# Kernel optimization log

Hardware: AMD Instinct MI355X
Metric: run time of the kernel (lower is better)

Reference implementation:

```python
import jax, jax.numpy as jnp
import numpy as np

N_NODES = 10000
N_EDGES = 50000
N_GRAPHS = 64
NODE_DIM = 32
EDGE_DIM = 16
HID = 64
EDGE_HID = 128
OUT_DIM = 1
T_STEPS = 3       # message-passing rounds
S2S_STEPS = 6     # Set2Set processing steps


def setup_inputs() -> dict:
    key = jax.random.key(0)
    ks = jax.random.split(key, 24)
    def w(k, shape, scale):
        return (jax.random.normal(k, shape, dtype=jnp.float32) * scale)
    inp = {}
    inp["node_features"] = jax.random.normal(ks[0], (N_NODES, NODE_DIM), dtype=jnp.float32)
    inp["edge_features"] = jax.random.normal(ks[1], (N_EDGES, EDGE_DIM), dtype=jnp.float32)
    inp["edge_index"] = jax.random.randint(ks[2], (2, N_EDGES), 0, N_NODES, dtype=jnp.int32)
    # sorted, fully-covering graph assignment (nodes of each graph are contiguous)
    inp["batch_indices"] = ((jnp.arange(N_NODES) * N_GRAPHS) // N_NODES).astype(jnp.int32)
    # input projection
    inp["W_proj"] = w(ks[3], (NODE_DIM, HID), 1.0 / np.sqrt(NODE_DIM))
    inp["b_proj"] = jnp.zeros((HID,), jnp.float32)
    # edge network MLP: edge_dim -> edge_hid -> hid*hid
    inp["W_e1"] = w(ks[4], (EDGE_DIM, EDGE_HID), 1.0 / np.sqrt(EDGE_DIM))
    inp["b_e1"] = jnp.zeros((EDGE_HID,), jnp.float32)
    inp["W_e2"] = w(ks[5], (EDGE_HID, HID * HID), 0.01)
    inp["b_e2"] = jnp.zeros((HID * HID,), jnp.float32)
    # GRU cell (torch layout: 3*hid rows = r,z,n)
    inp["W_gih"] = w(ks[6], (3 * HID, HID), 1.0 / np.sqrt(HID))
    inp["W_ghh"] = w(ks[7], (3 * HID, HID), 1.0 / np.sqrt(HID))
    inp["b_gih"] = jnp.zeros((3 * HID,), jnp.float32)
    inp["b_ghh"] = jnp.zeros((3 * HID,), jnp.float32)
    # LSTM cell (torch layout: 4*hid rows = i,f,g,o), input 2*hid
    inp["W_lih"] = w(ks[8], (4 * HID, 2 * HID), 1.0 / np.sqrt(HID))
    inp["W_lhh"] = w(ks[9], (4 * HID, HID), 1.0 / np.sqrt(HID))
    inp["b_lih"] = jnp.zeros((4 * HID,), jnp.float32)
    inp["b_lhh"] = jnp.zeros((4 * HID,), jnp.float32)
    # readout MLP: 2*hid -> hid -> out
    inp["W_m1"] = w(ks[10], (2 * HID, HID), 1.0 / np.sqrt(2 * HID))
    inp["b_m1"] = jnp.zeros((HID,), jnp.float32)
    inp["W_m2"] = w(ks[11], (HID, OUT_DIM), 1.0 / np.sqrt(HID))
    inp["b_m2"] = jnp.zeros((OUT_DIM,), jnp.float32)
    return inp


def _scatter_softmax(e, idx, n_seg):
    mx = jax.ops.segment_max(e, idx, num_segments=n_seg)
    ex = jnp.exp(e - mx[idx])
    s = jax.ops.segment_sum(ex, idx, num_segments=n_seg)
    return ex / (s[idx] + 1e-16)


def _mpnn_forward(node_features, edge_features, edge_index, batch_indices,
                  W_proj, b_proj, W_e1, b_e1, W_e2, b_e2,
                  W_gih, W_ghh, b_gih, b_ghh,
                  W_lih, W_lhh, b_lih, b_lhh,
                  W_m1, b_m1, W_m2, b_m2):
    n_nodes = node_features.shape[0]
    dst = edge_index[0]  # receiving node v
    src = edge_index[1]  # sending node w

    # input projection
    h = node_features @ W_proj + b_proj                       # (N, H)

    # edge network: per-edge transformation matrix A(e_vw) (depends only on edge feats)
    A = jax.nn.relu(edge_features @ W_e1 + b_e1) @ W_e2 + b_e2
    A = A.reshape(-1, HID, HID)                               # (E, H, H)

    # T rounds: gather senders, per-edge bmm, scatter-add to receivers, GRU update
    for _ in range(T_STEPS):
        msgs = jnp.einsum('eij,ej->ei', A, h[src])            # (E, H)
        m = jax.ops.segment_sum(msgs, dst, num_segments=n_nodes)
        gx = m @ W_gih.T + b_gih                              # (N, 3H)
        gh = h @ W_ghh.T + b_ghh
        xr, xz, xn = jnp.split(gx, 3, axis=-1)
        hr, hz, hn = jnp.split(gh, 3, axis=-1)
        r = jax.nn.sigmoid(xr + hr)
        z = jax.nn.sigmoid(xz + hz)
        n = jnp.tanh(xn + r * hn)
        h = (1.0 - z) * n + z * h

    # Set2Set readout
    hs = jnp.zeros((N_GRAPHS, HID), h.dtype)
    cs = jnp.zeros((N_GRAPHS, HID), h.dtype)
    rs = jnp.zeros((N_GRAPHS, HID), h.dtype)
    for _ in range(S2S_STEPS):
        q = hs[batch_indices]                                 # (N, H)
        e = jnp.sum(h * q, axis=-1)                           # (N,)
        a = _scatter_softmax(e, batch_indices, N_GRAPHS)
        rs = jax.ops.segment_sum(a[:, None] * h, batch_indices, num_segments=N_GRAPHS)
        x = jnp.concatenate([hs, rs], axis=-1)                # (G, 2H)
        gates = x @ W_lih.T + b_lih + hs @ W_lhh.T + b_lhh    # (G, 4H)
        i, f, g, o = jnp.split(gates, 4, axis=-1)
        cs = jax.nn.sigmoid(f) * cs + jax.nn.sigmoid(i) * jnp.tanh(g)
        hs = jax.nn.sigmoid(o) * jnp.tanh(cs)
    ge = jnp.concatenate([hs, rs], axis=-1)                   # (G, 2H)
    return jax.nn.relu(ge @ W_m1 + b_m1) @ W_m2 + b_m2        # (G, out)


def reference(node_features, edge_features, edge_index, batch_indices,
              W_proj, b_proj, W_e1, b_e1, W_e2, b_e2,
              W_gih, W_ghh, b_gih, b_ghh,
              W_lih, W_lhh, b_lih, b_lhh,
              W_m1, b_m1, W_m2, b_m2):
    return _mpnn_forward(node_features, edge_features, edge_index, batch_indices,
                         W_proj, b_proj, W_e1, b_e1, W_e2, b_e2,
                         W_gih, W_ghh, b_gih, b_ghh,
                         W_lih, W_lhh, b_lih, b_lhh,
                         W_m1, b_m1, W_m2, b_m2)
```

## Files before the change

### kernel.cpp

```cpp
#include <hip/hip_runtime.h>

#define N_NODES   10000
#define N_EDGES   50000
#define N_GRAPHS  64
#define NODE_DIM  32
#define EDGE_DIM  16
#define HID       64
#define EHID      128
#define T_STEPS   3
#define S2S_STEPS 6
#define TMB       5

typedef _Float16 half_t;
typedef _Float16 f16x8 __attribute__((ext_vector_type(8)));
typedef float    f32x4 __attribute__((ext_vector_type(4)));

__device__ __forceinline__ float sigf(float x){ return 1.0f/(1.0f + expf(-x)); }

__global__ void k_zero(float* p, int n){
  int i = blockIdx.x*256 + threadIdx.x;
  if (i < n) p[i] = 0.0f;
}

__global__ void k_proj(const float* __restrict__ nf, const float* __restrict__ Wp,
                       const float* __restrict__ bp, float* __restrict__ h){
  int idx = blockIdx.x*256 + threadIdx.x;
  if (idx >= N_NODES*HID) return;
  int n = idx >> 6;
  int c = idx & 63;
  float acc = bp[c];
  const float* row = nf + (size_t)n*NODE_DIM;
  for (int j = 0; j < NODE_DIM; ++j)
    acc = fmaf(row[j], Wp[j*HID + c], acc);
  h[idx] = acc;
}

__global__ void k_tw2(const float* __restrict__ W2, float* __restrict__ Mm){
  int idx = blockIdx.x*256 + threadIdx.x;
  if (idx >= 64*8192) return;
  int j = idx >> 13; int o = idx & 8191; int k = o >> 6; int i = o & 63;
  Mm[idx] = W2[(size_t)k*4096 + i*64 + j];
}

__global__ void k_w2bt(const float* __restrict__ W2, half_t* __restrict__ BT){
  int idx = blockIdx.x*256 + threadIdx.x;
  if (idx >= 512*2*64*8) return;
  int j    = idx & 7;
  int lane = (idx >> 3) & 63;
  int tk   = (idx >> 9) & 1;
  int tn   = idx >> 10;
  int k = tk*32 + ((lane >> 4) << 3) + j;
  int o = tn*16 + (lane & 15);
  BT[idx] = (half_t)W2[(size_t)(o >> 6)*4096 + (o & 63)*64 + k];
}

__global__ void k_prep(const float* __restrict__ h, const float* __restrict__ be2,
                       float* __restrict__ m, float* __restrict__ bhp,
                       half_t* __restrict__ AT){
  int idx = blockIdx.x*256 + threadIdx.x;
  if (idx >= N_NODES*HID) return;
  m[idx] = 0.0f;
  int n = idx >> 6, i = idx & 63;
  float acc = 0.0f;
  const float* row = be2 + (size_t)i*64;
  const float* hr  = h + (size_t)n*64;
  for (int j = 0; j < 64; ++j)
    acc = fmaf(row[j], hr[j], acc);
  bhp[idx] = acc;
  int j    = idx & 7;
  int lane = (idx >> 3) & 63;
  int tk   = (idx >> 9) & 1;
  int tm   = idx >> 10;
  int mrow = tm*16 + (lane & 15);
  int k    = tk*32 + ((lane >> 4) << 3) + j;
  AT[idx] = (half_t)h[(size_t)mrow*64 + k];
}

__global__ void k_twg(const float* __restrict__ Wg, const float* __restrict__ Wh,
                      float* __restrict__ WgT, float* __restrict__ WhT){
  int idx = blockIdx.x*256 + threadIdx.x;
  if (idx >= 192*64) return;
  int row = idx >> 6;
  int j   = idx & 63;
  WgT[j*192 + row] = Wg[(size_t)row*64 + j];
  WhT[j*192 + row] = Wh[(size_t)row*64 + j];
}

__global__ void k_ehid(const float* __restrict__ ef, const float* __restrict__ W1,
                       const float* __restrict__ b1, float* __restrict__ Hid){
  int idx = blockIdx.x*256 + threadIdx.x;
  if (idx >= N_EDGES*EHID) return;
  int e = idx >> 7, c = idx & 127;
  float acc = b1[c];
  const float* er = ef + (size_t)e*EDGE_DIM;
  for (int j = 0; j < EDGE_DIM; ++j)
    acc = fmaf(er[j], W1[j*EHID + c], acc);
  Hid[idx] = fmaxf(acc, 0.0f);
}

__global__ void k_ehid16(const float* __restrict__ ef, const float* __restrict__ W1,
                         const float* __restrict__ b1, half_t* __restrict__ Hid16){
  int idx = blockIdx.x*256 + threadIdx.x;
  if (idx >= N_EDGES*EHID) return;
  int e = idx >> 7, c = idx & 127;
  float acc = b1[c];
  const float* er = ef + (size_t)e*EDGE_DIM;
  for (int j = 0; j < EDGE_DIM; ++j)
    acc = fmaf(er[j], W1[j*EHID + c], acc);
  Hid16[idx] = (half_t)fmaxf(acc, 0.0f);
}

__global__ void k_bh(const float* __restrict__ h, const float* __restrict__ be2,
                     float* __restrict__ bh){
  int idx = blockIdx.x*256 + threadIdx.x;
  if (idx >= N_NODES*HID) return;
  int n = idx >> 6, i = idx & 63;
  float acc = 0.0f;
  const float* row = be2 + (size_t)i*64;
  const float* hr  = h + (size_t)n*64;
  for (int j = 0; j < 64; ++j)
    acc = fmaf(row[j], hr[j], acc);
  bh[idx] = acc;
}

__global__ void k_hist(const int* __restrict__ ids, int* __restrict__ deg){
  int e = blockIdx.x*256 + threadIdx.x;
  if (e >= N_EDGES) return;
  atomicAdd(&deg[ids[e]], 1);
}

__global__ void k_scan(const int* __restrict__ deg, int* __restrict__ rowptr,
                       int* __restrict__ cursor){
  __shared__ int part[256];
  int t = threadIdx.x;
  int base = t*40;
  int s = 0;
  for (int i = 0; i < 40; ++i){
    int idx = base + i;
    if (idx < N_NODES) s += deg[idx];
  }
  part[t] = s;
  __syncthreads();
  for (int off = 1; off < 256; off <<= 1){
    int v = (t >= off) ? part[t - off] : 0;
    __syncthreads();
    part[t] += v;
    __syncthreads();
  }
  int run = (t > 0) ? part[t - 1] : 0;
  for (int i = 0; i < 40; ++i){
    int idx = base + i;
    if (idx < N_NODES){
      rowptr[idx] = run;
      cursor[idx] = run;
      run += deg[idx];
    }
  }
  if (t == 255) rowptr[N_NODES] = run;
}

__global__ void k_scatter(const int* __restrict__ ids, int* __restrict__ cursor,
                          int* __restrict__ csr){
  int e = blockIdx.x*256 + threadIdx.x;
  if (e >= N_EDGES) return;
  int v = ids[e];
  int pos = atomicAdd(&cursor[v], 1);
  csr[pos] = e;
}

__global__ __launch_bounds__(256, 2)
void MPNN_55705725829535_kernel(const half_t* __restrict__ AT,
                                const half_t* __restrict__ BT,
                                const int* __restrict__ rowptr,
                                const int* __restrict__ csr,
                                const int* __restrict__ ei,
                                const half_t* __restrict__ Hid16,
                                const float* __restrict__ bh,
                                float* __restrict__ m){
  __shared__ half_t Ct[16][2][520];
  __shared__ int edgW[4][4][16];
  __shared__ int dstW[4][4][16];
  int wv   = threadIdx.x >> 6;
  int lane = threadIdx.x & 63;
  int quad = lane >> 4;
  int colb = lane & 15;
  int tmg = blockIdx.x;
  int q   = blockIdx.y;
  int kh  = blockIdx.z;

  f16x8 B0r[2][8], B1r[2][8];
  #pragma unroll
  for (int ktl = 0; ktl < 2; ++ktl)
    #pragma unroll
    for (int jj = 0; jj < 8; ++jj){
      int ke = (kh*2 + ktl)*32 + wv*8 + jj;
      const f16x8* Bb = (const f16x8*)BT + (size_t)(ke*4 + q)*128;
      B0r[ktl][jj] = Bb[lane];
      B1r[ktl][jj] = Bb[64 + lane];
    }

  for (int tt = 0; tt < TMB; ++tt){
    int tm = tmg*TMB + tt;
    const f16x8* Ab = (const f16x8*)AT + (size_t)tm*128;
    f16x8 a0 = Ab[lane];
    f16x8 a1 = Ab[64 + lane];

    {
      int nodeL = wv*4 + quad;
      int sL = tm*16 + nodeL;
      int begL = rowptr[sL];
      int endL = rowptr[sL + 1];
      int eL = (colb < endL - begL) ? csr[begL + colb] : -1;
      edgW[wv][quad][colb] = eL;
      dstW[wv][quad][colb] = (eL >= 0) ? ei[eL] : -1;
    }

    #pragma unroll
    for (int ktl = 0; ktl < 2; ++ktl){
      f32x4 acc[8];
      #pragma unroll
      for (int jj = 0; jj < 8; ++jj){
        acc[jj][0]=0.f; acc[jj][1]=0.f; acc[jj][2]=0.f; acc[jj][3]=0.f;
      }
      #pragma unroll
      for (int jj = 0; jj < 8; ++jj){
        acc[jj] = __builtin_amdgcn_mfma_f32_16x16x32_f16(a0, B0r[ktl][jj], acc[jj], 0, 0, 0);
        acc[jj] = __builtin_amdgcn_mfma_f32_16x16x32_f16(a1, B1r[ktl][jj], acc[jj], 0, 0, 0);
      }
      #pragma unroll
      for (int r = 0; r < 4; ++r){
        int node = quad*4 + r;
        f16x8 v;
        #pragma unroll
        for (int jj = 0; jj < 8; ++jj) v[jj] = (half_t)acc[jj][r];
        *(f16x8*)&Ct[node][ktl][(wv*16 + colb)*8] = v;
      }
    }
    __syncthreads();

    for (int c = 0; c < 4; ++c){
      int node = wv*4 + c;
      int s = tm*16 + node;
      int beg  = rowptr[s];
      int endp = rowptr[s + 1];
      if (beg == endp) continue;
      f16x8 B0 = *(const f16x8*)&Ct[node][0][lane*8];
      f16x8 B1 = *(const f16x8*)&Ct[node][1][lane*8];
      float bhc = (kh == 0) ? bh[(size_t)s*64 + q*16 + colb] : 0.0f;
      int gn0 = endp - beg; if (gn0 > 16) gn0 = 16;
      {
        f16x8 A0, A1;
        int e = (colb < gn0) ? edgW[wv][c][colb] : -1;
        if (e >= 0){
          const f16x8* Hb = (const f16x8*)(Hid16 + (size_t)e*128) + quad;
          A0 = Hb[(kh*2 + 0)*4];
          A1 = Hb[(kh*2 + 1)*4];
        } else {
          #pragma unroll
          for (int p = 0; p < 8; ++p){ A0[p] = (half_t)0; A1[p] = (half_t)0; }
        }
        f32x4 acc;
        acc[0]=0.f; acc[1]=0.f; acc[2]=0.f; acc[3]=0.f;
        acc = __builtin_amdgcn_mfma_f32_16x16x32_f16(A0, B0, acc, 0, 0, 0);
        acc = __builtin_amdgcn_mfma_f32_16x16x32_f16(A1, B1, acc, 0, 0, 0);
        #pragma unroll
        for (int r = 0; r < 4; ++r){
          int jrow = quad*4 + r;
          if (jrow < gn0){
            int d = dstW[wv][c][jrow];
            atomicAdd(&m[(size_t)d*64 + q*16 + colb], acc[r] + bhc);
          }
        }
      }
      for (int gbeg = beg + 16; gbeg < endp; gbeg += 16){
        int gn = endp - gbeg; if (gn > 16) gn = 16;
        if (lane < 16){
          int e2 = (lane < gn) ? csr[gbeg + lane] : -1;
          edgW[wv][c][lane] = e2;
          dstW[wv][c][lane] = (e2 >= 0) ? ei[e2] : -1;
        }
        f16x8 A0, A1;
        int e = (colb < gn) ? edgW[wv][c][colb] : -1;
        if (e >= 0){
          const f16x8* Hb = (const f16x8*)(Hid16 + (size_t)e*128) + quad;
          A0 = Hb[(kh*2 + 0)*4];
          A1 = Hb[(kh*2 + 1)*4];
        } else {
          #pragma unroll
          for (int p = 0; p < 8; ++p){ A0[p] = (half_t)0; A1[p] = (half_t)0; }
        }
        f32x4 acc;
        acc[0]=0.f; acc[1]=0.f; acc[2]=0.f; acc[3]=0.f;
        acc = __builtin_amdgcn_mfma_f32_16x16x32_f16(A0, B0, acc, 0, 0, 0);
        acc = __builtin_amdgcn_mfma_f32_16x16x32_f16(A1, B1, acc, 0, 0, 0);
        #pragma unroll
        for (int r = 0; r < 4; ++r){
          int jrow = quad*4 + r;
          if (jrow < gn){
            int d = dstW[wv][c][jrow];
            atomicAdd(&m[(size_t)d*64 + q*16 + colb], acc[r] + bhc);
          }
        }
      }
    }
    __syncthreads();
  }
}

__global__ void k_cgemm(const float* __restrict__ h, const float* __restrict__ Mm,
                        half_t* __restrict__ C, int lo, int hi){
  __shared__ float hs[16][64];
  int n0 = lo + blockIdx.x*16;
  int o0 = blockIdx.y*256 + threadIdx.x;
  for (int idx = threadIdx.x; idx < 16*64; idx += 256){
    int nn = idx >> 6, j = idx & 63;
    int node = n0 + nn;
    hs[nn][j] = (node < hi) ? h[(size_t)node*64 + j] : 0.0f;
  }
  __syncthreads();
  float acc0[16], acc1[16];
  #pragma unroll
  for (int nn = 0; nn < 16; ++nn){ acc0[nn] = 0.0f; acc1[nn] = 0.0f; }
  for (int j4 = 0; j4 < 16; ++j4){
    const float* M0 = Mm + (size_t)(j4*4)*8192;
    float a0 = M0[o0],            b0 = M0[o0 + 4096];
    float a1 = M0[8192 + o0],     b1 = M0[8192 + o0 + 4096];
    float a2 = M0[2*8192 + o0],   b2 = M0[2*8192 + o0 + 4096];
    float a3 = M0[3*8192 + o0],   b3 = M0[3*8192 + o0 + 4096];
    #pragma unroll
    for (int nn = 0; nn < 16; ++nn){
      float4 hv = *(const float4*)&hs[nn][j4*4];
      acc0[nn] = fmaf(hv.x, a0, acc0[nn]);
      acc1[nn] = fmaf(hv.x, b0, acc1[nn]);
      acc0[nn] = fmaf(hv.y, a1, acc0[nn]);
      acc1[nn] = fmaf(hv.y, b1, acc1[nn]);
      acc0[nn] = fmaf(hv.z, a2, acc0[nn]);
      acc1[nn] = fmaf(hv.z, b2, acc1[nn]);
      acc0[nn] = fmaf(hv.w, a3, acc0[nn]);
      acc1[nn] = fmaf(hv.w, b3, acc1[nn]);
    }
  }
  #pragma unroll
  for (int nn = 0; nn < 16; ++nn){
    int node = n0 + nn;
    if (node < hi){
      half_t* Cr = C + (size_t)(node - lo)*8192;
      Cr[o0]        = (half_t)acc0[nn];
      Cr[o0 + 4096] = (half_t)acc1[nn];
    }
  }
}

__global__ void k_msg_csr(const int* __restrict__ rowptr,
                          const int* __restrict__ csr,
                          const int* __restrict__ ei,
                          const float* __restrict__ Hid,
                          const half_t* __restrict__ C,
                          const float* __restrict__ bh,
                          float* __restrict__ m, int lo, int hi){
  __shared__ float hidL[4][8][128];
  int wave = threadIdx.x >> 6;
  int lane = threadIdx.x & 63;
  int s = lo + blockIdx.x*4 + wave;
  if (s >= hi) return;
  int beg = rowptr[s];
  int endp = rowptr[s + 1];
  if (beg == endp) return;
  float bhv = bh[(size_t)s*64 + lane];
  const half_t* Cb = C + (size_t)(s - lo)*8192 + lane;
  float (*hl)[128] = hidL[wave];
  for (int gbeg = beg; gbeg < endp; gbeg += 8){
    int gn = endp - gbeg; if (gn > 8) gn = 8;
    int dsts[8];
    int e0 = csr[gbeg];
    #pragma unroll
    for (int j = 0; j < 8; ++j){
      int e = (j < gn) ? csr[gbeg + j] : e0;
      dsts[j] = ei[e];
      hl[j][lane]      = Hid[(size_t)e*128 + lane];
      hl[j][lane + 64] = Hid[(size_t)e*128 + 64 + lane];
    }
    float acc[8];
    #pragma unroll
    for (int j = 0; j < 8; ++j) acc[j] = 0.0f;
    #pragma unroll 4
    for (int k = 0; k < 128; ++k){
      float c = (float)Cb[k*64];
      #pragma unroll
      for (int j = 0; j < 8; ++j)
        acc[j] = fmaf(hl[j][k], c, acc[j]);
    }
    for (int j = 0; j < gn; ++j)
      atomicAdd(&m[(size_t)dsts[j]*64 + lane], acc[j] + bhv);
  }
}

__global__ void k_msg_fb(const int* __restrict__ ei, const float* __restrict__ ef,
                         const float* __restrict__ W1, const float* __restrict__ b1,
                         const float* __restrict__ W2, const float* __restrict__ be2,
                         const float* __restrict__ h, float* __restrict__ m){
  __shared__ float HidL[EHID];
  __shared__ __align__(16) float hsL[HID];
  int e = blockIdx.x;
  int t = threadIdx.x;
  int src = ei[N_EDGES + e];
  int dst = ei[e];
  {
    float a0 = b1[t];
    float a1 = b1[t + 64];
    const float* er = ef + (size_t)e*EDGE_DIM;
    for (int j = 0; j < EDGE_DIM; ++j){
      float ev = er[j];
      a0 = fmaf(ev, W1[j*EHID + t],      a0);
      a1 = fmaf(ev, W1[j*EHID + t + 64], a1);
    }
    HidL[t]      = fmaxf(a0, 0.0f);
    HidL[t + 64] = fmaxf(a1, 0.0f);
    hsL[t] = h[(size_t)src*64 + t];
  }
  __syncthreads();
  float acc = 0.0f;
  for (int k = 0; k < EHID; ++k){
    float s = HidL[k];
    if (s != 0.0f){
      const float* w = W2 + (size_t)k*4096 + t*64;
      float partial = 0.0f;
      for (int j = 0; j < 64; ++j)
        partial = fmaf(hsL[j], w[j], partial);
      acc = fmaf(s, partial, acc);
    }
  }
  {
    const float* w = be2 + (size_t)t*64;
    for (int j = 0; j < 64; ++j)
      acc = fmaf(hsL[j], w[j], acc);
  }
  atomicAdd(&m[(size_t)dst*64 + t], acc);
}

__global__ void k_gru(float* __restrict__ h, const float* __restrict__ m,
                      const float* __restrict__ WgT, const float* __restrict__ WhT,
                      const float* __restrict__ bg, const float* __restrict__ bhb){
  __shared__ float mld[16][64];
  __shared__ float hld[16][64];
  int t  = threadIdx.x;
  int i  = t & 63;
  int wv = t >> 6;
  int n0 = blockIdx.x*16;
  for (int idx = t; idx < 16*64; idx += 256){
    int nn = idx >> 6, j = idx & 63;
    int node = n0 + nn;
    mld[nn][j] = m[(size_t)node*64 + j];
    hld[nn][j] = h[(size_t)node*64 + j];
  }
  __syncthreads();
  float xr[4], xz[4], xn[4], hr[4], hz[4], hn[4];
  #pragma unroll
  for (int c = 0; c < 4; ++c){
    xr[c] = bg[i];  xz[c] = bg[64 + i];  xn[c] = bg[128 + i];
    hr[c] = bhb[i]; hz[c] = bhb[64 + i]; hn[c] = bhb[128 + i];
  }
  for (int j = 0; j < 64; ++j){
    const float* wg = WgT + j*192;
    const float* wh = WhT + j*192;
    float wgr = wg[i], wgz = wg[64 + i], wgn = wg[128 + i];
    float whr = wh[i], whz = wh[64 + i], whn = wh[128 + i];
    #pragma unroll
    for (int c = 0; c < 4; ++c){
      int nn = wv*4 + c;
      float mj = mld[nn][j];
      float hj = hld[nn][j];
      xr[c] = fmaf(mj, wgr, xr[c]);
      xz[c] = fmaf(mj, wgz, xz[c]);
      xn[c] = fmaf(mj, wgn, xn[c]);
      hr[c] = fmaf(hj, whr, hr[c]);
      hz[c] = fmaf(hj, whz, hz[c]);
      hn[c] = fmaf(hj, whn, hn[c]);
    }
  }
  #pragma unroll
  for (int c = 0; c < 4; ++c){
    int nn = wv*4 + c;
    float r  = sigf(xr[c] + hr[c]);
    float z  = sigf(xz[c] + hz[c]);
    float nv = tanhf(xn[c] + r*hn[c]);
    h[(size_t)(n0 + nn)*64 + i] = (1.0f - z)*nv + z*hld[nn][i];
  }
}

__global__ void k_s2s(const float* __restrict__ h,
                      const float* __restrict__ Wli, const float* __restrict__ Wlh,
                      const float* __restrict__ bli, const float* __restrict__ blh,
                      const float* __restrict__ Wm1, const float* __restrict__ bm1,
                      const float* __restrict__ Wm2, const float* __restrict__ bm2,
                      float* __restrict__ out){
  __shared__ float hc[157*65];
  __shared__ float ea[160];
  __shared__ float x[192];
  __shared__ float gpart[512];
  __shared__ float rsp[8][64];
  __shared__ float wredA[8];
  __shared__ float wredB[8];
  __shared__ float hsb[64];
  __shared__ float csb[64];
  __shared__ float rsb[64];
  int g = blockIdx.x;
  int t = threadIdx.x;
  int lane = t & 63;
  int wv   = t >> 6;
  int start = (g*N_NODES + 63) >> 6;
  int end   = ((g + 1)*N_NODES + 63) >> 6;
  int cnt = end - start;
  const float* hg = h + (size_t)start*64;
  for (int idx = t; idx < cnt*64; idx += 512)
    hc[(idx >> 6)*65 + (idx & 63)] = hg[idx];
  if (t < 64){ hsb[t] = 0.0f; csb[t] = 0.0f; rsb[t] = 0.0f; }
  __syncthreads();
  for (int step = 0; step < S2S_STEPS; ++step){
    float ev = -1e30f;
    if (t < cnt){
      float a = 0.0f;
      const float* hr = &hc[t*65];
      for (int i = 0; i < 64; ++i) a = fmaf(hr[i], hsb[i], a);
      ev = a;
    }
    float v = ev;
    for (int o = 32; o > 0; o >>= 1) v = fmaxf(v, __shfl_xor(v, o));
    if (lane == 0) wredA[wv] = v;
    __syncthreads();
    float mx = wredA[0];
    #pragma unroll
    for (int i = 1; i < 8; ++i) mx = fmaxf(mx, wredA[i]);
    float ex = (t < cnt) ? expf(ev - mx) : 0.0f;
    float sv = ex;
    for (int o = 32; o > 0; o >>= 1) sv += __shfl_xor(sv, o);
    if (lane == 0) wredB[wv] = sv;
    __syncthreads();
    float ssum = 0.0f;
    #pragma unroll
    for (int i = 0; i < 8; ++i) ssum += wredB[i];
    if (t < cnt) ea[t] = ex / (ssum + 1e-16f);
    __syncthreads();
    {
      int n0 = wv*20;
      int n1 = n0 + 20; if (n1 > cnt) n1 = cnt;
      float r = 0.0f;
      for (int n = n0; n < n1; ++n)
        r = fmaf(ea[n], hc[n*65 + lane], r);
      rsp[wv][lane] = r;
    }
    __syncthreads();
    if (t < 64){
      float r = rsp[0][t] + rsp[1][t] + rsp[2][t] + rsp[3][t]
              + rsp[4][t] + rsp[5][t] + rsp[6][t] + rsp[7][t];
      rsb[t] = r;
      x[t]        = hsb[t];
      x[64 + t]   = r;
      x[128 + t]  = hsb[t];
    }
    __syncthreads();
    {
      int gate = t & 255;
      int half = t >> 8;
      float gl = 0.0f;
      if (half == 0){
        const float* wr = Wli + (size_t)gate*128;
        for (int jj = 0; jj < 96; ++jj) gl = fmaf(x[jj], wr[jj], gl);
      } else {
        const float* wr = Wli + (size_t)gate*128;
        for (int jj = 96; jj < 128; ++jj) gl = fmaf(x[jj], wr[jj], gl);
        const float* wh = Wlh + (size_t)gate*64;
        for (int jj = 0; jj < 64; ++jj) gl = fmaf(x[128 + jj], wh[jj], gl);
      }
      gpart[t] = gl;
    }
    __syncthreads();
    if (t < 64){
      float iv = sigf (gpart[t]       + gpart[t + 256]       + bli[t]       + blh[t]);
      float fv = sigf (gpart[64 + t]  + gpart[64 + t + 256]  + bli[64 + t]  + blh[64 + t]);
      float gv = tanhf(gpart[128 + t] + gpart[128 + t + 256] + bli[128 + t] + blh[128 + t]);
      float ov = sigf (gpart[192 + t] + gpart[192 + t + 256] + bli[192 + t] + blh[192 + t]);
      float c  = fv*csb[t] + iv*gv;
      csb[t] = c;
      hsb[t] = ov*tanhf(c);
    }
    __syncthreads();
  }
  float rv = 0.0f;
  if (t < 64){
    float v = bm1[t];
    for (int j = 0; j < 64; ++j) v = fmaf(hsb[j], Wm1[(size_t)j*64 + t],        v);
    for (int j = 0; j < 64; ++j) v = fmaf(rsb[j], Wm1[(size_t)(64 + j)*64 + t], v);
    v = fmaxf(v, 0.0f);
    rv = v * Wm2[t];
  }
  for (int o = 32; o > 0; o >>= 1) rv += __shfl_xor(rv, o);
  if (lane == 0) wredA[wv] = rv;
  __syncthreads();
  if (t == 0) out[g] = wredA[0] + wredA[1] + wredA[2] + wredA[3]
                     + wredA[4] + wredA[5] + wredA[6] + wredA[7] + bm2[0];
}

extern "C" void kernel_launch(void* const* d_in, const int* in_sizes, int n_in,
                              void* d_out, int out_size, void* d_ws, size_t ws_size,
                              hipStream_t stream){
  (void)in_sizes; (void)n_in; (void)out_size;

  const float* nf  = (const float*)d_in[0];
  const float* ef  = (const float*)d_in[1];
  const int*   ei  = (const int*)d_in[2];
  const float* Wp  = (const float*)d_in[4];
  const float* bp  = (const float*)d_in[5];
  const float* We1 = (const float*)d_in[6];
  const float* be1 = (const float*)d_in[7];
  const float* We2 = (const float*)d_in[8];
  const float* be2 = (const float*)d_in[9];
  const float* Wg  = (const float*)d_in[10];
  const float* Wh  = (const float*)d_in[11];
  const float* bg  = (const float*)d_in[12];
  const float* bhb = (const float*)d_in[13];
  const float* Wli = (const float*)d_in[14];
  const float* Wlh = (const float*)d_in[15];
  const float* bli = (const float*)d_in[16];
  const float* blh = (const float*)d_in[17];
  const float* Wm1 = (const float*)d_in[18];
  const float* bm1 = (const float*)d_in[19];
  const float* Wm2 = (const float*)d_in[20];
  const float* bm2 = (const float*)d_in[21];

  float* out = (float*)d_out;
  float* ws  = (float*)d_ws;

  float* h    = ws;
  float* m    = ws + 640000;
  float* bh   = ws + 1280000;
  float* Mm   = ws + 1920000;
  float* WgT  = ws + 2444288;
  float* WhT  = ws + 2456576;
  float* Hid  = ws + 2468864;
  half_t* Hid16 = (half_t*)Hid;
  int*   deg    = (int*)(ws + 8868864);
  int*   rowptr = deg + 10000;
  int*   cursor = rowptr + 10001;
  int*   csr    = cursor + 10000;
  half_t* AT  = (half_t*)(ws + 8948880);
  half_t* BT  = (half_t*)(ws + 9268880);
  const size_t C_OFF = 9531024;
  half_t* C   = (half_t*)(ws + C_OFF);

  long long c_halves = ((long long)ws_size - (long long)C_OFF*4) / 2;
  int NC = (c_halves > 0) ? (int)(c_halves / 8192) : 0;
  if (NC > N_NODES) NC = N_NODES;
  int use_c_path = (NC >= 512);
  int use_mfma   = (NC >= N_NODES);

  k_proj<<<(N_NODES*HID + 255)/256, 256, 0, stream>>>(nf, Wp, bp, h);

  if (use_c_path){
    k_twg <<<(192*64 + 255)/256, 256, 0, stream>>>(Wg, Wh, WgT, WhT);
    k_zero<<<(10000 + 255)/256, 256, 0, stream>>>((float*)deg, 10000);
    k_hist<<<(N_EDGES + 255)/256, 256, 0, stream>>>(ei + N_EDGES, deg);
    k_scan<<<1, 256, 0, stream>>>(deg, rowptr, cursor);
    k_scatter<<<(N_EDGES + 255)/256, 256, 0, stream>>>(ei + N_EDGES, cursor, csr);
    if (use_mfma){
      k_ehid16<<<(N_EDGES*EHID + 255)/256, 256, 0, stream>>>(ef, We1, be1, Hid16);
      k_w2bt<<<(512*2*64*8 + 255)/256, 256, 0, stream>>>(We2, BT);
      for (int step = 0; step < T_STEPS; ++step){
        k_prep<<<(N_NODES*HID + 255)/256, 256, 0, stream>>>(h, be2, m, bh, AT);
        dim3 grid(625/TMB, 4, 2);
        MPNN_55705725829535_kernel<<<grid, 256, 0, stream>>>(
            AT, BT, rowptr, csr, ei, Hid16, bh, m);
        k_gru<<<625, 256, 0, stream>>>(h, m, WgT, WhT, bg, bhb);
      }
    } else {
      k_ehid<<<(N_EDGES*EHID + 255)/256, 256, 0, stream>>>(ef, We1, be1, Hid);
      k_tw2<<<(64*8192)/256, 256, 0, stream>>>(We2, Mm);
      for (int step = 0; step < T_STEPS; ++step){
        k_zero<<<(N_NODES*HID + 255)/256, 256, 0, stream>>>(m, N_NODES*HID);
        k_bh<<<(N_NODES*HID + 255)/256, 256, 0, stream>>>(h, be2, bh);
        for (int lo = 0; lo < N_NODES; lo += NC){
          int hi = (lo + NC < N_NODES) ? lo + NC : N_NODES;
          int cnt = hi - lo;
          dim3 grid((cnt + 15)/16, 16);
          k_cgemm<<<grid, 256, 0, stream>>>(h, Mm, C, lo, hi);
          k_msg_csr<<<(cnt + 3)/4, 256, 0, stream>>>(
              rowptr, csr, ei, Hid, C, bh, m, lo, hi);
        }
        k_gru<<<625, 256, 0, stream>>>(h, m, WgT, WhT, bg, bhb);
      }
    }
  } else {
    k_twg <<<(192*64 + 255)/256, 256, 0, stream>>>(Wg, Wh, WgT, WhT);
    for (int step = 0; step < T_STEPS; ++step){
      k_zero<<<(N_NODES*HID + 255)/256, 256, 0, stream>>>(m, N_NODES*HID);
      k_msg_fb<<<N_EDGES, 64, 0, stream>>>(ei, ef, We1, be1, We2, be2, h, m);
      k_gru<<<625, 256, 0, stream>>>(h, m, WgT, WhT, bg, bhb);
    }
  }
  k_s2s<<<N_GRAPHS, 512, 0, stream>>>(h, Wli, Wlh, bli, blh,
                                      Wm1, bm1, Wm2, bm2, out);
}
```

Measured before the change: 547.4 us.

## Fuse projection/GRU with next-step prep and merge setup kernels into one launch

Merges the input projection with the per-step prep (zeroing m, computing the bias term bh and the fp16 MFMA operand AT), and fuses the GRU update with the next step's prep so h stays in shared memory. The one-time setup kernels (edge hidden layer, W2 transpose, GRU weight transpose, degree zeroing) become a single block-partitioned launch. The MFMA message kernel also prefetches the first edge-group Hid16 operands for all four nodes before the C-tile GEMM. Together these cut launch count and redundant global reads of h, at the cost of more register pressure in the message kernel and an extra bh/AT computation after the final step that nothing uses.

```diff
diff --git a/kernel.cpp b/kernel.cpp
--- a/kernel.cpp
+++ b/kernel.cpp
@@ -20,6 +20,98 @@
 __global__ void k_zero(float* p, int n){
   int i = blockIdx.x*256 + threadIdx.x;
   if (i < n) p[i] = 0.0f;
+}
+
+__global__ void k_proj_prep(const float* __restrict__ nf, const float* __restrict__ Wp,
+                            const float* __restrict__ bp, const float* __restrict__ be2,
+                            float* __restrict__ h, float* __restrict__ m,
+                            float* __restrict__ bh, half_t* __restrict__ AT){
+  __shared__ float hl[16][64];
+  int tm = blockIdx.x;
+  int t  = threadIdx.x;
+  #pragma unroll
+  for (int s = 0; s < 4; ++s){
+    int idx = t + s*256;
+    int ln = idx >> 6, c = idx & 63;
+    int n  = tm*16 + ln;
+    float acc = bp[c];
+    const float* row = nf + (size_t)n*NODE_DIM;
+    for (int j = 0; j < NODE_DIM; ++j)
+      acc = fmaf(row[j], Wp[j*HID + c], acc);
+    hl[ln][c] = acc;
+    h[(size_t)n*64 + c] = acc;
+    m[(size_t)n*64 + c] = 0.0f;
+  }
+  __syncthreads();
+  #pragma unroll
+  for (int s = 0; s < 4; ++s){
+    int idx = t + s*256;
+    int ln = idx >> 6, i = idx & 63;
+    int n  = tm*16 + ln;
+    float acc = 0.0f;
+    const float* row = be2 + (size_t)i*64;
+    for (int j = 0; j < 64; ++j)
+      acc = fmaf(row[j], hl[ln][j], acc);
+    bh[(size_t)n*64 + i] = acc;
+    int j8   = idx & 7;
+    int lane = (idx >> 3) & 63;
+    int tk   = (idx >> 9) & 1;
+    int k    = tk*32 + ((lane >> 4) << 3) + j8;
+    AT[(size_t)tm*1024 + idx] = (half_t)hl[lane & 15][k];
+  }
+}
+
+__global__ void k_tw2(const float* __restrict__ W2, float* __restrict__ Mm){
+  int idx = blockIdx.x*256 + threadIdx.x;
+  if (idx >= 64*8192) return;
+  int j = idx >> 13; int o = idx & 8191; int k = o >> 6; int i = o & 63;
+  Mm[idx] = W2[(size_t)k*4096 + i*64 + j];
+}
+
+__global__ void k_setup0(const float* __restrict__ ef, const float* __restrict__ W1,
+                         const float* __restrict__ b1, half_t* __restrict__ Hid16,
+                         const float* __restrict__ W2, half_t* __restrict__ BT,
+                         const float* __restrict__ Wg, const float* __restrict__ Wh,
+                         float* __restrict__ WgT, float* __restrict__ WhT,
+                         int* __restrict__ deg){
+  int b = blockIdx.x;
+  if (b < 25000){
+    int idx = b*256 + threadIdx.x;
+    int e = idx >> 7, c = idx & 127;
+    float acc = b1[c];
+    const float* er = ef + (size_t)e*EDGE_DIM;
+    for (int j = 0; j < EDGE_DIM; ++j)
+      acc = fmaf(er[j], W1[j*EHID + c], acc);
+    Hid16[idx] = (half_t)fmaxf(acc, 0.0f);
+  } else if (b < 27048){
+    int idx = (b - 25000)*256 + threadIdx.x;
+    int j    = idx & 7;
+    int lane = (idx >> 3) & 63;
+    int tk   = (idx >> 9) & 1;
+    int tn   = idx >> 10;
+    int k = tk*32 + ((lane >> 4) << 3) + j;
+    int o = tn*16 + (lane & 15);
+    BT[idx] = (half_t)W2[(size_t)(o >> 6)*4096 + (o & 63)*64 + k];
+  } else if (b < 27096){
+    int idx = (b - 27048)*256 + threadIdx.x;
+    int row = idx >> 6;
+    int j   = idx & 63;
+    WgT[j*192 + row] = Wg[(size_t)row*64 + j];
+    WhT[j*192 + row] = Wh[(size_t)row*64 + j];
+  } else {
+    int idx = (b - 27096)*256 + threadIdx.x;
+    if (idx < 10000) deg[idx] = 0;
+  }
+}
+
+__global__ void k_twg(const float* __restrict__ Wg, const float* __restrict__ Wh,
+                      float* __restrict__ WgT, float* __restrict__ WhT){
+  int idx = blockIdx.x*256 + threadIdx.x;
+  if (idx >= 192*64) return;
+  int row = idx >> 6;
+  int j   = idx & 63;
+  WgT[j*192 + row] = Wg[(size_t)row*64 + j];
+  WhT[j*192 + row] = Wh[(size_t)row*64 + j];
 }
 
 __global__ void k_proj(const float* __restrict__ nf, const float* __restrict__ Wp,
@@ -35,57 +127,6 @@
   h[idx] = acc;
 }
 
-__global__ void k_tw2(const float* __restrict__ W2, float* __restrict__ Mm){
-  int idx = blockIdx.x*256 + threadIdx.x;
-  if (idx >= 64*8192) return;
-  int j = idx >> 13; int o = idx & 8191; int k = o >> 6; int i = o & 63;
-  Mm[idx] = W2[(size_t)k*4096 + i*64 + j];
-}
-
-__global__ void k_w2bt(const float* __restrict__ W2, half_t* __restrict__ BT){
-  int idx = blockIdx.x*256 + threadIdx.x;
-  if (idx >= 512*2*64*8) return;
-  int j    = idx & 7;
-  int lane = (idx >> 3) & 63;
-  int tk   = (idx >> 9) & 1;
-  int tn   = idx >> 10;
-  int k = tk*32 + ((lane >> 4) << 3) + j;
-  int o = tn*16 + (lane & 15);
-  BT[idx] = (half_t)W2[(size_t)(o >> 6)*4096 + (o & 63)*64 + k];
-}
-
-__global__ void k_prep(const float* __restrict__ h, const float* __restrict__ be2,
-                       float* __restrict__ m, float* __restrict__ bhp,
-                       half_t* __restrict__ AT){
-  int idx = blockIdx.x*256 + threadIdx.x;
-  if (idx >= N_NODES*HID) return;
-  m[idx] = 0.0f;
-  int n = idx >> 6, i = idx & 63;
-  float acc = 0.0f;
-  const float* row = be2 + (size_t)i*64;
-  const float* hr  = h + (size_t)n*64;
-  for (int j = 0; j < 64; ++j)
-    acc = fmaf(row[j], hr[j], acc);
-  bhp[idx] = acc;
-  int j    = idx & 7;
-  int lane = (idx >> 3) & 63;
-  int tk   = (idx >> 9) & 1;
-  int tm   = idx >> 10;
-  int mrow = tm*16 + (lane & 15);
-  int k    = tk*32 + ((lane >> 4) << 3) + j;
-  AT[idx] = (half_t)h[(size_t)mrow*64 + k];
-}
-
-__global__ void k_twg(const float* __restrict__ Wg, const float* __restrict__ Wh,
-                      float* __restrict__ WgT, float* __restrict__ WhT){
-  int idx = blockIdx.x*256 + threadIdx.x;
-  if (idx >= 192*64) return;
-  int row = idx >> 6;
-  int j   = idx & 63;
-  WgT[j*192 + row] = Wg[(size_t)row*64 + j];
-  WhT[j*192 + row] = Wh[(size_t)row*64 + j];
-}
-
 __global__ void k_ehid(const float* __restrict__ ef, const float* __restrict__ W1,
                        const float* __restrict__ b1, float* __restrict__ Hid){
   int idx = blockIdx.x*256 + threadIdx.x;
@@ -96,18 +137,6 @@
   for (int j = 0; j < EDGE_DIM; ++j)
     acc = fmaf(er[j], W1[j*EHID + c], acc);
   Hid[idx] = fmaxf(acc, 0.0f);
-}
-
-__global__ void k_ehid16(const float* __restrict__ ef, const float* __restrict__ W1,
-                         const float* __restrict__ b1, half_t* __restrict__ Hid16){
-  int idx = blockIdx.x*256 + threadIdx.x;
-  if (idx >= N_EDGES*EHID) return;
-  int e = idx >> 7, c = idx & 127;
-  float acc = b1[c];
-  const float* er = ef + (size_t)e*EDGE_DIM;
-  for (int j = 0; j < EDGE_DIM; ++j)
-    acc = fmaf(er[j], W1[j*EHID + c], acc);
-  Hid16[idx] = (half_t)fmaxf(acc, 0.0f);
 }
 
 __global__ void k_bh(const float* __restrict__ h, const float* __restrict__ be2,
@@ -214,6 +243,19 @@
       edgW[wv][quad][colb] = eL;
       dstW[wv][quad][colb] = (eL >= 0) ? ei[eL] : -1;
     }
+    f16x8 Ap0[4], Ap1[4];
+    #pragma unroll
+    for (int c = 0; c < 4; ++c){
+      int e = edgW[wv][c][colb];
+      if (e >= 0){
+        const f16x8* Hb = (const f16x8*)(Hid16 + (size_t)e*128) + quad;
+        Ap0[c] = Hb[(kh*2 + 0)*4];
+        Ap1[c] = Hb[(kh*2 + 1)*4];
+      } else {
+        #pragma unroll
+        for (int p = 0; p < 8; ++p){ Ap0[c][p] = (half_t)0; Ap1[c][p] = (half_t)0; }
+      }
+    }
 
     #pragma unroll
     for (int ktl = 0; ktl < 2; ++ktl){
@@ -249,20 +291,10 @@
       float bhc = (kh == 0) ? bh[(size_t)s*64 + q*16 + colb] : 0.0f;
       int gn0 = endp - beg; if (gn0 > 16) gn0 = 16;
       {
-        f16x8 A0, A1;
-        int e = (colb < gn0) ? edgW[wv][c][colb] : -1;
-        if (e >= 0){
-          const f16x8* Hb = (const f16x8*)(Hid16 + (size_t)e*128) + quad;
-          A0 = Hb[(kh*2 + 0)*4];
-          A1 = Hb[(kh*2 + 1)*4];
-        } else {
-          #pragma unroll
-          for (int p = 0; p < 8; ++p){ A0[p] = (half_t)0; A1[p] = (half_t)0; }
-        }
         f32x4 acc;
         acc[0]=0.f; acc[1]=0.f; acc[2]=0.f; acc[3]=0.f;
-        acc = __builtin_amdgcn_mfma_f32_16x16x32_f16(A0, B0, acc, 0, 0, 0);
-        acc = __builtin_amdgcn_mfma_f32_16x16x32_f16(A1, B1, acc, 0, 0, 0);
+        acc = __builtin_amdgcn_mfma_f32_16x16x32_f16(Ap0[c], B0, acc, 0, 0, 0);
+        acc = __builtin_amdgcn_mfma_f32_16x16x32_f16(Ap1[c], B1, acc, 0, 0, 0);
         #pragma unroll
         for (int r = 0; r < 4; ++r){
           int jrow = quad*4 + r;
@@ -488,6 +520,84 @@
   }
 }
 
+__global__ void k_gru_prep(float* __restrict__ h, float* __restrict__ m,
+                           const float* __restrict__ WgT, const float* __restrict__ WhT,
+                           const float* __restrict__ bg, const float* __restrict__ bhb,
+                           const float* __restrict__ be2,
+                           float* __restrict__ bh, half_t* __restrict__ AT){
+  __shared__ float mld[16][64];
+  __shared__ float hld[16][64];
+  int t  = threadIdx.x;
+  int i  = t & 63;
+  int wv = t >> 6;
+  int n0 = blockIdx.x*16;
+  for (int idx = t; idx < 16*64; idx += 256){
+    int nn = idx >> 6, j = idx & 63;
+    int node = n0 + nn;
+    mld[nn][j] = m[(size_t)node*64 + j];
+    hld[nn][j] = h[(size_t)node*64 + j];
+    m[(size_t)node*64 + j] = 0.0f;
+  }
+  __syncthreads();
+  float xr[4], xz[4], xn[4], hr[4], hz[4], hn[4];
+  #pragma unroll
+  for (int c = 0; c < 4; ++c){
+    xr[c] = bg[i];  xz[c] = bg[64 + i];  xn[c] = bg[128 + i];
+    hr[c] = bhb[i]; hz[c] = bhb[64 + i]; hn[c] = bhb[128 + i];
+  }
+  for (int j = 0; j < 64; ++j){
+    const float* wg = WgT + j*192;
+    const float* wh = WhT + j*192;
+    float wgr = wg[i], wgz = wg[64 + i], wgn = wg[128 + i];
+    float whr = wh[i], whz = wh[64 + i], whn = wh[128 + i];
+    #pragma unroll
+    for (int c = 0; c < 4; ++c){
+      int nn = wv*4 + c;
+      float mj = mld[nn][j];
+      float hj = hld[nn][j];
+      xr[c] = fmaf(mj, wgr, xr[c]);
+      xz[c] = fmaf(mj, wgz, xz[c]);
+      xn[c] = fmaf(mj, wgn, xn[c]);
+      hr[c] = fmaf(hj, whr, hr[c]);
+      hz[c] = fmaf(hj, whz, hz[c]);
+      hn[c] = fmaf(hj, whn, hn[c]);
+    }
+  }
+  float hnew[4];
+  #pragma unroll
+  for (int c = 0; c < 4; ++c){
+    int nn = wv*4 + c;
+    float r  = sigf(xr[c] + hr[c]);
+    float z  = sigf(xz[c] + hz[c]);
+    float nv = tanhf(xn[c] + r*hn[c]);
+    hnew[c] = (1.0f - z)*nv + z*hld[nn][i];
+  }
+  __syncthreads();
+  #pragma unroll
+  for (int c = 0; c < 4; ++c){
+    int nn = wv*4 + c;
+    hld[nn][i] = hnew[c];
+    h[(size_t)(n0 + nn)*64 + i] = hnew[c];
+  }
+  __syncthreads();
+  #pragma unroll
+  for (int s = 0; s < 4; ++s){
+    int idx = t + s*256;
+    int ln = idx >> 6, ii = idx & 63;
+    int node = n0 + ln;
+    float acc = 0.0f;
+    const float* row = be2 + (size_t)ii*64;
+    for (int j = 0; j < 64; ++j)
+      acc = fmaf(row[j], hld[ln][j], acc);
+    bh[(size_t)node*64 + ii] = acc;
+    int j8   = idx & 7;
+    int lane = (idx >> 3) & 63;
+    int tk   = (idx >> 9) & 1;
+    int k    = tk*32 + ((lane >> 4) << 3) + j8;
+    AT[(size_t)blockIdx.x*1024 + idx] = (half_t)hld[lane & 15][k];
+  }
+}
+
 __global__ void k_s2s(const float* __restrict__ h,
                       const float* __restrict__ Wli, const float* __restrict__ Wlh,
                       const float* __restrict__ bli, const float* __restrict__ blh,
@@ -654,42 +764,43 @@
   int use_c_path = (NC >= 512);
   int use_mfma   = (NC >= N_NODES);
 
-  k_proj<<<(N_NODES*HID + 255)/256, 256, 0, stream>>>(nf, Wp, bp, h);
-
-  if (use_c_path){
+  if (use_c_path && use_mfma){
+    k_proj_prep<<<625, 256, 0, stream>>>(nf, Wp, bp, be2, h, m, bh, AT);
+    k_setup0<<<27136, 256, 0, stream>>>(ef, We1, be1, Hid16, We2, BT,
+                                        Wg, Wh, WgT, WhT, deg);
+    k_hist<<<(N_EDGES + 255)/256, 256, 0, stream>>>(ei + N_EDGES, deg);
+    k_scan<<<1, 256, 0, stream>>>(deg, rowptr, cursor);
+    k_scatter<<<(N_EDGES + 255)/256, 256, 0, stream>>>(ei + N_EDGES, cursor, csr);
+    for (int step = 0; step < T_STEPS; ++step){
+      dim3 grid(625/TMB, 4, 2);
+      MPNN_55705725829535_kernel<<<grid, 256, 0, stream>>>(
+          AT, BT, rowptr, csr, ei, Hid16, bh, m);
+      k_gru_prep<<<625, 256, 0, stream>>>(h, m, WgT, WhT, bg, bhb, be2, bh, AT);
+    }
+  } else if (use_c_path){
+    k_proj<<<(N_NODES*HID + 255)/256, 256, 0, stream>>>(nf, Wp, bp, h);
     k_twg <<<(192*64 + 255)/256, 256, 0, stream>>>(Wg, Wh, WgT, WhT);
     k_zero<<<(10000 + 255)/256, 256, 0, stream>>>((float*)deg, 10000);
     k_hist<<<(N_EDGES + 255)/256, 256, 0, stream>>>(ei + N_EDGES, deg);
     k_scan<<<1, 256, 0, stream>>>(deg, rowptr, cursor);
     k_scatter<<<(N_EDGES + 255)/256, 256, 0, stream>>>(ei + N_EDGES, cursor, csr);
-    if (use_mfma){
-      k_ehid16<<<(N_EDGES*EHID + 255)/256, 256, 0, stream>>>(ef, We1, be1, Hid16);
-      k_w2bt<<<(512*2*64*8 + 255)/256, 256, 0, stream>>>(We2, BT);
-      for (int step = 0; step < T_STEPS; ++step){
-        k_prep<<<(N_NODES*HID + 255)/256, 256, 0, stream>>>(h, be2, m, bh, AT);
-        dim3 grid(625/TMB, 4, 2);
-        MPNN_55705725829535_kernel<<<grid, 256, 0, stream>>>(
-            AT, BT, rowptr, csr, ei, Hid16, bh, m);
-        k_gru<<<625, 256, 0, stream>>>(h, m, WgT, WhT, bg, bhb);
+    k_ehid<<<(N_EDGES*EHID + 255)/256, 256, 0, stream>>>(ef, We1, be1, Hid);
+    k_tw2<<<(64*8192)/256, 256, 0, stream>>>(We2, Mm);
+    for (int step = 0; step < T_STEPS; ++step){
+      k_zero<<<(N_NODES*HID + 255)/256, 256, 0, stream>>>(m, N_NODES*HID);
+      k_bh<<<(N_NODES*HID + 255)/256, 256, 0, stream>>>(h, be2, bh);
+      for (int lo = 0; lo < N_NODES; lo += NC){
+        int hi = (lo + NC < N_NODES) ? lo + NC : N_NODES;
+        int cnt = hi - lo;
+        dim3 grid((cnt + 15)/16, 16);
+        k_cgemm<<<grid, 256, 0, stream>>>(h, Mm, C, lo, hi);
+        k_msg_csr<<<(cnt + 3)/4, 256, 0, stream>>>(
+            rowptr, csr, ei, Hid, C, bh, m, lo, hi);
       }
-    } else {
-      k_ehid<<<(N_EDGES*EHID + 255)/256, 256, 0, stream>>>(ef, We1, be1, Hid);
-      k_tw2<<<(64*8192)/256, 256, 0, stream>>>(We2, Mm);
-      for (int step = 0; step < T_STEPS; ++step){
-        k_zero<<<(N_NODES*HID + 255)/256, 256, 0, stream>>>(m, N_NODES*HID);
-        k_bh<<<(N_NODES*HID + 255)/256, 256, 0, stream>>>(h, be2, bh);
-        for (int lo = 0; lo < N_NODES; lo += NC){
-          int hi = (lo + NC < N_NODES) ? lo + NC : N_NODES;
-          int cnt = hi - lo;
-          dim3 grid((cnt + 15)/16, 16);
-          k_cgemm<<<grid, 256, 0, stream>>>(h, Mm, C, lo, hi);
-          k_msg_csr<<<(cnt + 3)/4, 256, 0, stream>>>(
-              rowptr, csr, ei, Hid, C, bh, m, lo, hi);
-        }
-        k_gru<<<625, 256, 0, stream>>>(h, m, WgT, WhT, bg, bhb);
-      }
+      k_gru<<<625, 256, 0, stream>>>(h, m, WgT, WhT, bg, bhb);
     }
   } else {
+    k_proj<<<(N_NODES*HID + 255)/256, 256, 0, stream>>>(nf, Wp, bp, h);
     k_twg <<<(192*64 + 255)/256, 256, 0, stream>>>(Wg, Wh, WgT, WhT);
     for (int step = 0; step < T_STEPS; ++step){
       k_zero<<<(N_NODES*HID + 255)/256, 256, 0, stream>>>(m, N_NODES*HID);
```

New measurement: 759.3 us. 38.7% more time.
